# Optimization experiments

Hardware: AMD Instinct MI355X
Metric: run time of the kernel (lower is better)

The kernel has to match this reference:

```python
import jax, jax.numpy as jnp
import numpy as np

PASS = 8        # pass_through_size
FLOW = 16       # flow_size
TRANS = FLOW - PASS  # transform_size = 8
NBINS = 64
HID = 1024


def _conditioner(yA, w1, b1, w2, b2, w3, b3):
    # MLP producing unnormalized positive bin widths Q: [B, TRANS, NBINS]
    h = jax.nn.relu(yA @ w1 + b1)
    h = jax.nn.relu(h @ w2 + b2)
    q = jax.nn.softplus(h @ w3 + b3) + 1e-6  # positivity for slopes
    return q.reshape(-1, TRANS, NBINS)


def setup_inputs() -> dict:
    key = jax.random.key(0)
    ks = jax.random.split(key, 4)
    B = 65536
    y = jax.random.uniform(ks[0], (B, FLOW + 1), dtype=jnp.float32)
    w1 = jax.random.normal(ks[1], (PASS, HID), dtype=jnp.float32) / np.sqrt(PASS)
    w2 = jax.random.normal(ks[2], (HID, HID), dtype=jnp.float32) / np.sqrt(HID)
    w3 = jax.random.normal(ks[3], (HID, TRANS * NBINS), dtype=jnp.float32) / np.sqrt(HID)
    return {
        "y": y,
        "w1": w1, "b1": jnp.zeros((HID,), jnp.float32),
        "w2": w2, "b2": jnp.zeros((HID,), jnp.float32),
        "w3": w3, "b3": jnp.zeros((TRANS * NBINS,), jnp.float32),
    }


def reference(y, w1, b1, w2, b2, w3, b3):
    yA = y[:, :PASS]                      # [B, PASS]
    yB = y[:, PASS:FLOW]                  # [B, TRANS]
    jac = y[:, FLOW:FLOW + 1]             # [B, 1]

    Q = _conditioner(yA, w1, b1, w2, b2, w3, b3)  # [B, TRANS, NBINS]
    Qsum = jnp.cumsum(Q, axis=-1)
    Qnorms = Qsum[:, :, -1:]
    Q = Q / (Qnorms / NBINS)              # slopes per bin
    Qsum = Qsum / Qnorms                  # normalized CDF knots (last == 1)

    # searchsorted(side='left') per row: count of knots strictly below value
    ybins = jnp.sum(Qsum < yB[..., None], axis=-1)          # [B, TRANS] int32
    ybins = jnp.clip(ybins, 0, NBINS - 1)                   # guard fp edge case

    paddedQsum = jnp.pad(Qsum, ((0, 0), (0, 0), (1, 0)))    # prepend 0 knot
    offsets = jnp.take_along_axis(paddedQsum, ybins[..., None], axis=-1)[..., 0]
    slopes = jnp.take_along_axis(Q, ybins[..., None], axis=-1)[..., 0]

    xB = (yB - offsets) / slopes + ybins.astype(jnp.float32) / NBINS
    jac = jac * jnp.prod(1.0 / slopes, axis=-1, keepdims=True)
    return jnp.concatenate((yA, xB, jac), axis=-1)          # [B, FLOW+1]
```

## Files before the change

### kernel.cpp

```cpp
#include <hip/hip_runtime.h>
#include <hip/hip_fp16.h>

#define HID 1024
#define QCOLS 512
#define KP 2048
#define NT 48

typedef _Float16 f16x8 __attribute__((ext_vector_type(8)));
typedef float f32x4 __attribute__((ext_vector_type(4)));

__global__ void tconv_split(const float* __restrict__ src, __half* __restrict__ dst,
                            int K, int N, float scale) {
  __shared__ float tile[32][33];
  int n0 = blockIdx.x * 32, k0 = blockIdx.y * 32;
  int tx = threadIdx.x, ty = threadIdx.y;
  for (int i = ty; i < 32; i += 8)
    tile[i][tx] = src[(size_t)(k0 + i) * N + n0 + tx];
  __syncthreads();
  for (int i = ty; i < 32; i += 8) {
    float v = tile[tx][i] * scale;
    __half h = __float2half(v);
    size_t o = (size_t)(n0 + i) * (2 * K) + k0 + tx;
    dst[o] = h;
    dst[o + K] = __float2half(v - __half2float(h));
  }
}

__global__ __launch_bounds__(256)
void h1_split_v2(const float* __restrict__ y, const float* __restrict__ w1,
                 const float* __restrict__ b1, __half* __restrict__ h1,
                 int row0, int nrows) {
  const int t = threadIdx.x & 127;
  const int rl = threadIdx.x >> 7;
  const long r = (long)blockIdx.x * 2 + rl;
  if (r >= nrows) return;
  const float* yr = y + (size_t)(row0 + r) * 17;
  float yv[8];
#pragma unroll
  for (int k = 0; k < 8; ++k) yv[k] = yr[k];
  const int c0 = t * 8;
  f32x4 a0 = *(const f32x4*)(b1 + c0);
  f32x4 a1 = *(const f32x4*)(b1 + c0 + 4);
#pragma unroll
  for (int k = 0; k < 8; ++k) {
    const f32x4 w0 = *(const f32x4*)(w1 + k * HID + c0);
    const f32x4 w1v = *(const f32x4*)(w1 + k * HID + c0 + 4);
#pragma unroll
    for (int j = 0; j < 4; ++j) {
      a0[j] = fmaf(yv[k], w0[j], a0[j]);
      a1[j] = fmaf(yv[k], w1v[j], a1[j]);
    }
  }
  f16x8 hi, lo;
#pragma unroll
  for (int j = 0; j < 8; ++j) {
    float v = fmaxf(j < 4 ? a0[j] : a1[j - 4], 0.f) * 64.f;
    _Float16 h = (_Float16)v;
    hi[j] = h;
    lo[j] = (_Float16)(v - (float)h);
  }
  *(f16x8*)(h1 + (size_t)r * KP + c0) = hi;
  *(f16x8*)(h1 + (size_t)r * KP + c0 + 1024) = lo;
}

template <int ACT>
__device__ __forceinline__
void gemm8p_body(const __half* __restrict__ A, const __half* __restrict__ B,
                 const float* __restrict__ bias, __half* __restrict__ Co,
                 float* __restrict__ Cf, int ldc) {
  __shared__ char lds[131072];
  const int tid = threadIdx.x;
  const int lane = tid & 63, wave = tid >> 6;
  const int p = lane & 15, ql = lane >> 4;
  const int wm = wave >> 2, wn = wave & 3;

  const int gx = gridDim.x, nwg = gx * gridDim.y;
  const int bid = blockIdx.y * gx + blockIdx.x;
  const int q8 = nwg >> 3, r8 = nwg & 7;
  const int xcd = bid & 7, lxi = bid >> 3;
  const int swz = (xcd < r8 ? xcd * (q8 + 1) : r8 * (q8 + 1) + (xcd - r8) * q8) + lxi;
  const size_t row_blk = (size_t)(swz / gx) * 256;
  const size_t col_blk = (size_t)(swz % gx) * 256;

  int a_off[8], b_off[4];
#pragma unroll
  for (int m = 0; m < 8; ++m) {
    int r = wm * 128 + m * 16 + p;
    a_off[m] = r * 64 + ((ql ^ ((r >> 1) & 3)) << 4);
  }
#pragma unroll
  for (int n = 0; n < 4; ++n) {
    int r = wn * 64 + n * 16 + p;
    b_off[n] = r * 64 + ((ql ^ ((r >> 1) & 3)) << 4);
  }

  const int idx0 = tid, idx1 = tid + 512;
  const int sr0 = idx0 >> 2, sq0 = (idx0 & 3) ^ ((sr0 >> 1) & 3);
  const int sr1 = idx1 >> 2, sq1 = (idx1 & 3) ^ ((sr1 >> 1) & 3);

  auto stage = [&](int buf, int h, int kt) {
    const int lk = kt * 64;
    const int ak = ((lk >= 2048) ? 1024 : 0) + (lk & 1023) + h * 32;
    const int bk = ((lk >= 1024 && lk < 2048) ? 1024 : 0) + (lk & 1023) + h * 32;
    char* pa = lds + buf * 65536 + h * 16384;
    char* pb = pa + 32768;
    const __half* ga0 = A + (row_blk + sr0) * (size_t)KP + ak + sq0 * 8;
    const __half* ga1 = A + (row_blk + sr1) * (size_t)KP + ak + sq1 * 8;
    const __half* gb0 = B + (col_blk + sr0) * (size_t)KP + bk + sq0 * 8;
    const __half* gb1 = B + (col_blk + sr1) * (size_t)KP + bk + sq1 * 8;
    __builtin_amdgcn_global_load_lds((__attribute__((address_space(1))) void*)ga0,
        (__attribute__((address_space(3))) void*)(pa + idx0 * 16), 16, 0, 0);
    __builtin_amdgcn_global_load_lds((__attribute__((address_space(1))) void*)ga1,
        (__attribute__((address_space(3))) void*)(pa + idx1 * 16), 16, 0, 0);
    __builtin_amdgcn_global_load_lds((__attribute__((address_space(1))) void*)gb0,
        (__attribute__((address_space(3))) void*)(pb + idx0 * 16), 16, 0, 0);
    __builtin_amdgcn_global_load_lds((__attribute__((address_space(1))) void*)gb1,
        (__attribute__((address_space(3))) void*)(pb + idx1 * 16), 16, 0, 0);
  };

  stage(0, 0, 0);
  stage(0, 1, 0);
  asm volatile("s_waitcnt vmcnt(0)" ::: "memory");
  __builtin_amdgcn_s_barrier();

  f32x4 acc[8][4] = {};

  for (int t = 0; t < NT; ++t) {
    const int bufp = t & 1;
    const int ts = (t + 1 < NT) ? t + 1 : NT - 1;
#pragma unroll
    for (int h = 0; h < 2; ++h) {
      const char* pA = lds + bufp * 65536 + h * 16384;
      const char* pB = pA + 32768;
      f16x8 af[8], bfr[4];
#pragma unroll
      for (int m = 0; m < 8; ++m) af[m] = *(const f16x8*)(pA + a_off[m]);
#pragma unroll
      for (int n = 0; n < 4; ++n) bfr[n] = *(const f16x8*)(pB + b_off[n]);
      stage(bufp ^ 1, h, ts);
      __builtin_amdgcn_sched_barrier(0);
      __builtin_amdgcn_s_barrier();
      __builtin_amdgcn_sched_barrier(0);
      __builtin_amdgcn_s_setprio(1);
#pragma unroll
      for (int m = 0; m < 8; ++m)
#pragma unroll
        for (int n = 0; n < 4; ++n)
          acc[m][n] = __builtin_amdgcn_mfma_f32_16x16x32_f16(af[m], bfr[n], acc[m][n], 0, 0, 0);
      __builtin_amdgcn_s_setprio(0);
      asm volatile("s_waitcnt vmcnt(4)" ::: "memory");
      __builtin_amdgcn_sched_barrier(0);
      __builtin_amdgcn_s_barrier();
      __builtin_amdgcn_sched_barrier(0);
    }
  }

  const float unscale = 1.f / 16384.f;
#pragma unroll
  for (int n = 0; n < 4; ++n) {
    const size_t col = col_blk + wn * 64 + n * 16 + p;
    const float bv = bias[col];
#pragma unroll
    for (int m = 0; m < 8; ++m) {
      const size_t row0 = row_blk + wm * 128 + m * 16 + ql * 4;
#pragma unroll
      for (int j = 0; j < 4; ++j) {
        float v = acc[m][n][j] * unscale + bv;
        const size_t o = (row0 + j) * (size_t)ldc + col;
        if constexpr (ACT == 0) {
          float r = fmaxf(v, 0.f) * 64.f;
          __half hh = __float2half(r);
          Co[o] = hh;
          Co[o + 1024] = __float2half(r - __half2float(hh));
        } else {
          float sp = fmaxf(v, 0.f) + log1pf(expf(-fabsf(v)));
          Cf[o] = sp + 1e-6f;
        }
      }
    }
  }
}

__global__ __launch_bounds__(512, 2)
void gemm8p_relu(const __half* __restrict__ A, const __half* __restrict__ B,
                 const float* __restrict__ bias, __half* __restrict__ Co, int ldc) {
  gemm8p_body<0>(A, B, bias, Co, nullptr, ldc);
}

__global__ __launch_bounds__(512, 2)
void gemm8p_soft(const __half* __restrict__ A, const __half* __restrict__ B,
                 const float* __restrict__ bias, float* __restrict__ Cf, int ldc) {
  gemm8p_body<1>(A, B, bias, nullptr, Cf, ldc);
}

__global__ __launch_bounds__(256)
void pwl_epilogue(const float* __restrict__ y, const float* __restrict__ q,
                  float* __restrict__ out, int row0, int nrows) {
  const int wave = threadIdx.x >> 6, lane = threadIdx.x & 63;
  const int r = blockIdx.x * 4 + wave;
  if (r >= nrows) return;
  const float* yr = y + (size_t)(row0 + r) * 17;
  float* orow = out + (size_t)(row0 + r) * 17;
  const float* qr = q + (size_t)r * QCOLS;
  float prod_inv = 1.f;
#pragma unroll
  for (int t = 0; t < 8; ++t) {
    const float qv = qr[t * 64 + lane];
    float s = qv;
#pragma unroll
    for (int d = 1; d < 64; d <<= 1) {
      float u = __shfl_up(s, d);
      if (lane >= d) s += u;
    }
    const float total = __shfl(s, 63);
    const float sn = s / total;
    const float dnorm = total * 0.015625f;
    const float slope_l = qv / dnorm;
    const float yb = yr[8 + t];
    const unsigned long long m = __ballot(sn < yb);
    int bin = (int)__popcll(m);
    bin = bin > 63 ? 63 : bin;
    const float off_g = __shfl(sn, bin > 0 ? bin - 1 : 0);
    const float off = (bin == 0) ? 0.f : off_g;
    const float sl = __shfl(slope_l, bin);
    const float xB = (yb - off) / sl + (float)bin * 0.015625f;
    if (lane == t) orow[8 + t] = xB;
    prod_inv *= (1.f / sl);
  }
  if (lane < 8) orow[lane] = yr[lane];
  if (lane == 8) orow[16] = yr[16] * prod_inv;
}

extern "C" void kernel_launch(void* const* d_in, const int* in_sizes, int n_in,
                              void* d_out, int out_size, void* d_ws, size_t ws_size,
                              hipStream_t stream) {
  const float* y  = (const float*)d_in[0];
  const float* w1 = (const float*)d_in[1];
  const float* b1 = (const float*)d_in[2];
  const float* w2 = (const float*)d_in[3];
  const float* b2 = (const float*)d_in[4];
  const float* w3 = (const float*)d_in[5];
  const float* b3 = (const float*)d_in[6];
  float* out = (float*)d_out;
  const long Btot = in_sizes[0] / 17;

  char* ws = (char*)d_ws;
  __half* w2t = (__half*)ws;
  __half* w3t = (__half*)(ws + (4u << 20));
  const size_t fixed = (size_t)6 << 20;

  size_t avail = ws_size > fixed ? ws_size - fixed : 0;
  long maxrows = (long)(avail / 8192);
  long chunk = Btot < maxrows ? Btot : maxrows;
  chunk &= ~255L;
  if (chunk < 256) chunk = 256;

  __half* h1buf = (__half*)(ws + fixed);
  __half* h2buf = (__half*)(ws + fixed + (size_t)chunk * 4096);
  float* qbuf = (float*)h1buf;

  dim3 tb(32, 8);
  tconv_split<<<dim3(HID / 32, HID / 32), tb, 0, stream>>>(w2, w2t, HID, HID, 256.f);
  tconv_split<<<dim3(QCOLS / 32, HID / 32), tb, 0, stream>>>(w3, w3t, HID, QCOLS, 256.f);

  for (long row0 = 0; row0 < Btot; row0 += chunk) {
    const int nr = (int)((Btot - row0 < chunk) ? (Btot - row0) : chunk);
    h1_split_v2<<<(nr + 1) / 2, 256, 0, stream>>>(y, w1, b1, h1buf, (int)row0, nr);
    gemm8p_relu<<<dim3(HID / 256, nr / 256), 512, 0, stream>>>(h1buf, w2t, b2, h2buf, KP);
    gemm8p_soft<<<dim3(QCOLS / 256, nr / 256), 512, 0, stream>>>(h2buf, w3t, b3, qbuf, QCOLS);
    pwl_epilogue<<<(nr + 3) / 4, 256, 0, stream>>>(y, qbuf, out, (int)row0, nr);
  }
}
```

Baseline: 1.081 ms.

## Fuse third GEMM with softplus and piecewise-linear epilogue; merge weight conversions

The third GEMM now has each workgroup own a full 256-row block and loop over both 256-column halves. Softplus results are staged in LDS and the spline inversion runs in-kernel, with the per-row Jacobian product carried across halves through LDS. This removes the fp32 Q buffer round-trip through global memory and one kernel launch. The two weight transpose-conversion launches are merged into one grid using a z dimension. In exchange, the GEMM grid is halved, so there are fewer workgroups to fill the machine, and the serialized epilogue passes add barrier time inside the GEMM kernel.

```diff
diff --git a/kernel.cpp b/kernel.cpp
--- a/kernel.cpp
+++ b/kernel.cpp
@@ -9,27 +9,32 @@
 typedef _Float16 f16x8 __attribute__((ext_vector_type(8)));
 typedef float f32x4 __attribute__((ext_vector_type(4)));
 
-__global__ void tconv_split(const float* __restrict__ src, __half* __restrict__ dst,
-                            int K, int N, float scale) {
+__global__ void tconv_both(const float* __restrict__ w2, __half* __restrict__ w2t,
+                           const float* __restrict__ w3, __half* __restrict__ w3t) {
   __shared__ float tile[32][33];
+  const int z = blockIdx.z;
+  const int N = z ? QCOLS : HID;
+  if (blockIdx.x * 32 >= N) return;
+  const float* src = z ? w3 : w2;
+  __half* dst = z ? w3t : w2t;
   int n0 = blockIdx.x * 32, k0 = blockIdx.y * 32;
   int tx = threadIdx.x, ty = threadIdx.y;
   for (int i = ty; i < 32; i += 8)
     tile[i][tx] = src[(size_t)(k0 + i) * N + n0 + tx];
   __syncthreads();
   for (int i = ty; i < 32; i += 8) {
-    float v = tile[tx][i] * scale;
+    float v = tile[tx][i] * 256.f;
     __half h = __float2half(v);
-    size_t o = (size_t)(n0 + i) * (2 * K) + k0 + tx;
+    size_t o = (size_t)(n0 + i) * KP + k0 + tx;
     dst[o] = h;
-    dst[o + K] = __float2half(v - __half2float(h));
+    dst[o + 1024] = __float2half(v - __half2float(h));
   }
 }
 
 __global__ __launch_bounds__(256)
-void h1_split_v2(const float* __restrict__ y, const float* __restrict__ w1,
-                 const float* __restrict__ b1, __half* __restrict__ h1,
-                 int row0, int nrows) {
+void h1k(const float* __restrict__ y, const float* __restrict__ w1,
+         const float* __restrict__ b1, __half* __restrict__ h1,
+         int row0, int nrows) {
   const int t = threadIdx.x & 127;
   const int rl = threadIdx.x >> 7;
   const long r = (long)blockIdx.x * 2 + rl;
@@ -63,11 +68,9 @@
   *(f16x8*)(h1 + (size_t)r * KP + c0 + 1024) = lo;
 }
 
-template <int ACT>
-__device__ __forceinline__
-void gemm8p_body(const __half* __restrict__ A, const __half* __restrict__ B,
-                 const float* __restrict__ bias, __half* __restrict__ Co,
-                 float* __restrict__ Cf, int ldc) {
+__global__ __launch_bounds__(512, 2)
+void g2relu(const __half* __restrict__ A, const __half* __restrict__ B,
+            const float* __restrict__ bias, __half* __restrict__ Co) {
   __shared__ char lds[131072];
   const int tid = threadIdx.x;
   const int lane = tid & 63, wave = tid >> 6;
@@ -166,69 +169,177 @@
 #pragma unroll
       for (int j = 0; j < 4; ++j) {
         float v = acc[m][n][j] * unscale + bv;
-        const size_t o = (row0 + j) * (size_t)ldc + col;
-        if constexpr (ACT == 0) {
-          float r = fmaxf(v, 0.f) * 64.f;
-          __half hh = __float2half(r);
-          Co[o] = hh;
-          Co[o + 1024] = __float2half(r - __half2float(hh));
-        } else {
-          float sp = fmaxf(v, 0.f) + log1pf(expf(-fabsf(v)));
-          Cf[o] = sp + 1e-6f;
+        const size_t o = (row0 + j) * (size_t)KP + col;
+        float r = fmaxf(v, 0.f) * 64.f;
+        __half hh = __float2half(r);
+        Co[o] = hh;
+        Co[o + 1024] = __float2half(r - __half2float(hh));
+      }
+    }
+  }
+}
+
+__global__ __launch_bounds__(512, 2)
+void g3softepi(const __half* __restrict__ A, const __half* __restrict__ B,
+               const float* __restrict__ b3, const float* __restrict__ y,
+               float* __restrict__ out, int row0) {
+  __shared__ char lds[131072 + 1024];
+  float* qs = (float*)lds;
+  float* prod_lds = (float*)(lds + 131072);
+  const int tid = threadIdx.x;
+  const int lane = tid & 63, wave = tid >> 6;
+  const int p = lane & 15, ql = lane >> 4;
+  const int wm = wave >> 2, wn = wave & 3;
+
+  const int nwg = gridDim.x, bid = blockIdx.x;
+  const int q8 = nwg >> 3, r8 = nwg & 7;
+  const int xcd = bid & 7, lxi = bid >> 3;
+  const int swz = (xcd < r8 ? xcd * (q8 + 1) : r8 * (q8 + 1) + (xcd - r8) * q8) + lxi;
+  const size_t row_blk = (size_t)swz * 256;
+
+  int a_off[8], b_off[4];
+#pragma unroll
+  for (int m = 0; m < 8; ++m) {
+    int r = wm * 128 + m * 16 + p;
+    a_off[m] = r * 64 + ((ql ^ ((r >> 1) & 3)) << 4);
+  }
+#pragma unroll
+  for (int n = 0; n < 4; ++n) {
+    int r = wn * 64 + n * 16 + p;
+    b_off[n] = r * 64 + ((ql ^ ((r >> 1) & 3)) << 4);
+  }
+
+  const int idx0 = tid, idx1 = tid + 512;
+  const int sr0 = idx0 >> 2, sq0 = (idx0 & 3) ^ ((sr0 >> 1) & 3);
+  const int sr1 = idx1 >> 2, sq1 = (idx1 & 3) ^ ((sr1 >> 1) & 3);
+
+  const float unscale = 1.f / 16384.f;
+
+  for (int cb = 0; cb < 2; ++cb) {
+    const int col_blk = cb * 256;
+
+    auto stage = [&](int buf, int h, int kt) {
+      const int lk = kt * 64;
+      const int ak = ((lk >= 2048) ? 1024 : 0) + (lk & 1023) + h * 32;
+      const int bk = ((lk >= 1024 && lk < 2048) ? 1024 : 0) + (lk & 1023) + h * 32;
+      char* pa = lds + buf * 65536 + h * 16384;
+      char* pb = pa + 32768;
+      const __half* ga0 = A + (row_blk + sr0) * (size_t)KP + ak + sq0 * 8;
+      const __half* ga1 = A + (row_blk + sr1) * (size_t)KP + ak + sq1 * 8;
+      const __half* gb0 = B + (col_blk + sr0) * (size_t)KP + bk + sq0 * 8;
+      const __half* gb1 = B + (col_blk + sr1) * (size_t)KP + bk + sq1 * 8;
+      __builtin_amdgcn_global_load_lds((__attribute__((address_space(1))) void*)ga0,
+          (__attribute__((address_space(3))) void*)(pa + idx0 * 16), 16, 0, 0);
+      __builtin_amdgcn_global_load_lds((__attribute__((address_space(1))) void*)ga1,
+          (__attribute__((address_space(3))) void*)(pa + idx1 * 16), 16, 0, 0);
+      __builtin_amdgcn_global_load_lds((__attribute__((address_space(1))) void*)gb0,
+          (__attribute__((address_space(3))) void*)(pb + idx0 * 16), 16, 0, 0);
+      __builtin_amdgcn_global_load_lds((__attribute__((address_space(1))) void*)gb1,
+          (__attribute__((address_space(3))) void*)(pb + idx1 * 16), 16, 0, 0);
+    };
+
+    stage(0, 0, 0);
+    stage(0, 1, 0);
+    asm volatile("s_waitcnt vmcnt(0)" ::: "memory");
+    __builtin_amdgcn_s_barrier();
+
+    f32x4 acc[8][4] = {};
+
+    for (int t = 0; t < NT; ++t) {
+      const int bufp = t & 1;
+      const int ts = (t + 1 < NT) ? t + 1 : NT - 1;
+#pragma unroll
+      for (int h = 0; h < 2; ++h) {
+        const char* pA = lds + bufp * 65536 + h * 16384;
+        const char* pB = pA + 32768;
+        f16x8 af[8], bfr[4];
+#pragma unroll
+        for (int m = 0; m < 8; ++m) af[m] = *(const f16x8*)(pA + a_off[m]);
+#pragma unroll
+        for (int n = 0; n < 4; ++n) bfr[n] = *(const f16x8*)(pB + b_off[n]);
+        stage(bufp ^ 1, h, ts);
+        __builtin_amdgcn_sched_barrier(0);
+        __builtin_amdgcn_s_barrier();
+        __builtin_amdgcn_sched_barrier(0);
+        __builtin_amdgcn_s_setprio(1);
+#pragma unroll
+        for (int m = 0; m < 8; ++m)
+#pragma unroll
+          for (int n = 0; n < 4; ++n)
+            acc[m][n] = __builtin_amdgcn_mfma_f32_16x16x32_f16(af[m], bfr[n], acc[m][n], 0, 0, 0);
+        __builtin_amdgcn_s_setprio(0);
+        asm volatile("s_waitcnt vmcnt(4)" ::: "memory");
+        __builtin_amdgcn_sched_barrier(0);
+        __builtin_amdgcn_s_barrier();
+        __builtin_amdgcn_sched_barrier(0);
+      }
+    }
+
+    asm volatile("s_waitcnt vmcnt(0)" ::: "memory");
+    __syncthreads();
+
+    for (int pass = 0; pass < 4; ++pass) {
+      if (wm == (pass >> 1)) {
+#pragma unroll
+        for (int mm = 0; mm < 4; ++mm) {
+          const int m = (pass & 1) * 4 + mm;
+#pragma unroll
+          for (int n = 0; n < 4; ++n) {
+            const int colq = wn * 64 + n * 16 + p;
+            const float bv = b3[col_blk + colq];
+#pragma unroll
+            for (int j = 0; j < 4; ++j) {
+              float v = acc[m][n][j] * unscale + bv;
+              float sp = fmaxf(v, 0.f) + log1pf(expf(-fabsf(v)));
+              const int rloc = m * 16 + ql * 4 + j - (pass & 1) * 64;
+              qs[rloc * 256 + colq] = sp + 1e-6f;
+            }
+          }
         }
       }
-    }
-  }
-}
-
-__global__ __launch_bounds__(512, 2)
-void gemm8p_relu(const __half* __restrict__ A, const __half* __restrict__ B,
-                 const float* __restrict__ bias, __half* __restrict__ Co, int ldc) {
-  gemm8p_body<0>(A, B, bias, Co, nullptr, ldc);
-}
-
-__global__ __launch_bounds__(512, 2)
-void gemm8p_soft(const __half* __restrict__ A, const __half* __restrict__ B,
-                 const float* __restrict__ bias, float* __restrict__ Cf, int ldc) {
-  gemm8p_body<1>(A, B, bias, nullptr, Cf, ldc);
-}
-
-__global__ __launch_bounds__(256)
-void pwl_epilogue(const float* __restrict__ y, const float* __restrict__ q,
-                  float* __restrict__ out, int row0, int nrows) {
-  const int wave = threadIdx.x >> 6, lane = threadIdx.x & 63;
-  const int r = blockIdx.x * 4 + wave;
-  if (r >= nrows) return;
-  const float* yr = y + (size_t)(row0 + r) * 17;
-  float* orow = out + (size_t)(row0 + r) * 17;
-  const float* qr = q + (size_t)r * QCOLS;
-  float prod_inv = 1.f;
-#pragma unroll
-  for (int t = 0; t < 8; ++t) {
-    const float qv = qr[t * 64 + lane];
-    float s = qv;
-#pragma unroll
-    for (int d = 1; d < 64; d <<= 1) {
-      float u = __shfl_up(s, d);
-      if (lane >= d) s += u;
-    }
-    const float total = __shfl(s, 63);
-    const float sn = s / total;
-    const float dnorm = total * 0.015625f;
-    const float slope_l = qv / dnorm;
-    const float yb = yr[8 + t];
-    const unsigned long long m = __ballot(sn < yb);
-    int bin = (int)__popcll(m);
-    bin = bin > 63 ? 63 : bin;
-    const float off_g = __shfl(sn, bin > 0 ? bin - 1 : 0);
-    const float off = (bin == 0) ? 0.f : off_g;
-    const float sl = __shfl(slope_l, bin);
-    const float xB = (yb - off) / sl + (float)bin * 0.015625f;
-    if (lane == t) orow[8 + t] = xB;
-    prod_inv *= (1.f / sl);
-  }
-  if (lane < 8) orow[lane] = yr[lane];
-  if (lane == 8) orow[16] = yr[16] * prod_inv;
+      __syncthreads();
+
+      for (int i = 0; i < 8; ++i) {
+        const int rloc = wave * 8 + i;
+        const size_t rg = row0 + row_blk + pass * 64 + rloc;
+        const float* yr = y + rg * 17;
+        float* orow = out + rg * 17;
+        float prod = 1.f;
+#pragma unroll
+        for (int tl = 0; tl < 4; ++tl) {
+          const int t = cb * 4 + tl;
+          const float qv = qs[rloc * 256 + tl * 64 + lane];
+          float s = qv;
+#pragma unroll
+          for (int d = 1; d < 64; d <<= 1) {
+            float u = __shfl_up(s, d);
+            if (lane >= d) s += u;
+          }
+          const float total = __shfl(s, 63);
+          const float sn = s / total;
+          const float dnorm = total * 0.015625f;
+          const float slope_l = qv / dnorm;
+          const float yb = yr[8 + t];
+          const unsigned long long mb = __ballot(sn < yb);
+          int bin = (int)__popcll(mb);
+          bin = bin > 63 ? 63 : bin;
+          const float off_g = __shfl(sn, bin > 0 ? bin - 1 : 0);
+          const float off = (bin == 0) ? 0.f : off_g;
+          const float sl = __shfl(slope_l, bin);
+          const float xB = (yb - off) / sl + (float)bin * 0.015625f;
+          if (lane == t) orow[8 + t] = xB;
+          prod *= (1.f / sl);
+        }
+        if (cb == 0) {
+          if (lane == 0) prod_lds[pass * 64 + rloc] = prod;
+        } else {
+          if (lane < 8) orow[lane] = yr[lane];
+          if (lane == 8) orow[16] = yr[16] * prod_lds[pass * 64 + rloc] * prod;
+        }
+      }
+      __syncthreads();
+    }
+  }
 }
 
 extern "C" void kernel_launch(void* const* d_in, const int* in_sizes, int n_in,
@@ -257,17 +368,13 @@
 
   __half* h1buf = (__half*)(ws + fixed);
   __half* h2buf = (__half*)(ws + fixed + (size_t)chunk * 4096);
-  float* qbuf = (float*)h1buf;
-
-  dim3 tb(32, 8);
-  tconv_split<<<dim3(HID / 32, HID / 32), tb, 0, stream>>>(w2, w2t, HID, HID, 256.f);
-  tconv_split<<<dim3(QCOLS / 32, HID / 32), tb, 0, stream>>>(w3, w3t, HID, QCOLS, 256.f);
+
+  tconv_both<<<dim3(32, 32, 2), dim3(32, 8), 0, stream>>>(w2, w2t, w3, w3t);
 
   for (long row0 = 0; row0 < Btot; row0 += chunk) {
     const int nr = (int)((Btot - row0 < chunk) ? (Btot - row0) : chunk);
-    h1_split_v2<<<(nr + 1) / 2, 256, 0, stream>>>(y, w1, b1, h1buf, (int)row0, nr);
-    gemm8p_relu<<<dim3(HID / 256, nr / 256), 512, 0, stream>>>(h1buf, w2t, b2, h2buf, KP);
-    gemm8p_soft<<<dim3(QCOLS / 256, nr / 256), 512, 0, stream>>>(h2buf, w3t, b3, qbuf, QCOLS);
-    pwl_epilogue<<<(nr + 3) / 4, 256, 0, stream>>>(y, qbuf, out, (int)row0, nr);
-  }
-}
+    h1k<<<(nr + 1) / 2, 256, 0, stream>>>(y, w1, b1, h1buf, (int)row0, nr);
+    g2relu<<<dim3(HID / 256, nr / 256), 512, 0, stream>>>(h1buf, w2t, b2, h2buf);
+    g3softepi<<<nr / 256, 512, 0, stream>>>(h2buf, w3t, b3, y, out, (int)row0);
+  }
+}
```

New measurement: 2.062 ms. 1.91x slower.
